# Performance work log

Measured on AMD Instinct MI355X. Metric: run time of the kernel, lower is better.

## Reference

```python
import jax, jax.numpy as jnp
import numpy as np

N, K, D_IN, D_OUT = 50000, 16, 128, 256
C1, C2 = D_OUT // 4, D_OUT // 2  # 64, 128
E = N * K


def _lin(key, din, dout):
    return jax.random.normal(key, (din, dout), jnp.float32) * 0.02


def setup_inputs() -> dict:
    key = jax.random.key(0)
    ks = jax.random.split(key, 16)
    x = jax.random.normal(ks[0], (N, D_IN), jnp.float32)
    pos = jax.random.normal(ks[1], (N, 3), jnp.float32)
    normals = jax.random.normal(ks[2], (N, 3), jnp.float32)
    batch = jnp.zeros((N,), jnp.int32)
    # fixed k-regular graph standing in for knn_graph(pos, K); src != dst so
    # darboux's sqrt(|pos_j-pos_i|^2) is smooth everywhere
    dst = jnp.repeat(jnp.arange(N, dtype=jnp.int32), K)            # [E]
    off = jax.random.randint(ks[3], (E,), 1, N, jnp.int32)
    src = (dst + off) % N                                          # [E]
    edge_index = jnp.stack([src, dst])                             # [2,E]
    inp = dict(x=x, pos=pos, batch=batch, normals=normals, edge_index=edge_index)

    def add_mlp(name, k, din, dout):
        inp[name + '_w'] = _lin(k, din, dout)
        inp[name + '_b'] = jnp.zeros((dout,), jnp.float32)
        inp[name + '_g'] = jnp.ones((dout,), jnp.float32)
        inp[name + '_bt'] = jnp.zeros((dout,), jnp.float32)

    add_mlp('mlp1', ks[4], D_IN, D_OUT // 8)
    add_mlp('sc', ks[5], D_IN, D_OUT)
    add_mlp('mlp2', ks[6], C2, D_OUT)
    add_mlp('enc1', ks[7], 8, C1 // 2)
    inp['att1_w'] = _lin(ks[8], C1, C1)
    add_mlp('post1', ks[9], C1, C1)
    add_mlp('enc2', ks[10], 8, C2 // 2)
    inp['att2_w'] = _lin(ks[11], C2, C2)
    add_mlp('post2', ks[12], C2, C2)
    return inp


def _bn(h, g, bt, eps=1e-6):
    # BatchNorm1d, training-mode batch statistics (biased variance)
    m = h.mean(0)
    v = jnp.mean((h - m) ** 2, axis=0)
    return (h - m) * jax.lax.rsqrt(v + eps) * g + bt


def _lrelu(h):
    return jnp.where(h >= 0, h, 0.2 * h)


def _smlp(h, w, b, g, bt, act=True):
    # SharedMLP layer: Linear -> BN(eps=1e-6) -> LeakyReLU(0.2) (act optional)
    h = _bn(h @ w + b, g, bt)
    return _lrelu(h) if act else h


def _darboux(pi, pj, ni, nj):
    eps = 1e-10
    d = pj - pi                                            # [E,3]
    dot = lambda a, b: jnp.sum(a * b, axis=1, keepdims=True)
    nrm = lambda a: jnp.sqrt(jnp.sum(a * a, axis=1, keepdims=True))
    dist = nrm(d)
    lni, lnj = nrm(ni), nrm(nj)
    uq = jnp.cross(d, ni); vq = jnp.cross(uq, ni)
    uk = jnp.cross(d, nj); vk = jnp.cross(uk, nj)
    luq, lvq, luk, lvk = nrm(uq), nrm(vq), nrm(uk), nrm(vk)
    return jnp.concatenate([
        dist,
        dot(d, ni) / (dist * lni + eps),
        dot(d, nj) / (dist * lnj + eps),
        dot(ni, nj) / (lni * lnj + eps),
        dot(uq, uk) / (luq * luk + eps),
        dot(vq, vk) / (lvq * lvk + eps),
        dot(uq, vk) / (luq * lvk + eps),
        dot(vq, uk) / (lvq * luk + eps),
    ], axis=1)                                             # [E,8]


def _seg_softmax(h, idx, n):
    m = jax.ops.segment_max(h, idx, num_segments=n)        # [N,C]
    e = jnp.exp(h - m[idx])
    s = jax.ops.segment_sum(e, idx, num_segments=n)
    return e / (s[idx] + 1e-16)


def _lfa(src, dst, n, x, pos, normals, ew, eb, eg, ebt, aw, pw, pb, pg, pbt):
    rel = _darboux(pos[dst], pos[src], normals[dst], normals[src])  # [E,8]
    lse = _smlp(rel, ew, eb, eg, ebt)                               # [E,C/2]
    lf = jnp.concatenate([x[src], lse], axis=1)                     # [E,C]
    att = lf @ aw                                                   # [E,C]
    scores = _seg_softmax(att, dst, n)
    agg = jax.ops.segment_sum(scores * lf, dst, num_segments=n)     # [N,C]
    return _smlp(agg, pw, pb, pg, pbt)


def reference(x, pos, batch, normals, edge_index,
              mlp1_w, mlp1_b, mlp1_g, mlp1_bt,
              sc_w, sc_b, sc_g, sc_bt,
              mlp2_w, mlp2_b, mlp2_g, mlp2_bt,
              enc1_w, enc1_b, enc1_g, enc1_bt, att1_w,
              post1_w, post1_b, post1_g, post1_bt,
              enc2_w, enc2_b, enc2_g, enc2_bt, att2_w,
              post2_w, post2_b, post2_g, post2_bt):
    n = x.shape[0]
    src, dst = edge_index[0], edge_index[1]
    shortcut = _smlp(x, sc_w, sc_b, sc_g, sc_bt, act=False)         # [N,d_out]
    h = _smlp(x, mlp1_w, mlp1_b, mlp1_g, mlp1_bt)                   # [N,d_out//8]
    h = _lfa(src, dst, n, h, pos, normals,
             enc1_w, enc1_b, enc1_g, enc1_bt, att1_w,
             post1_w, post1_b, post1_g, post1_bt)                   # [N,d_out//4]
    h = _lfa(src, dst, n, h, pos, normals,
             enc2_w, enc2_b, enc2_g, enc2_bt, att2_w,
             post2_w, post2_b, post2_g, post2_bt)                   # [N,d_out//2]
    h = _smlp(h, mlp2_w, mlp2_b, mlp2_g, mlp2_bt, act=False)        # [N,d_out]
    return _lrelu(h + shortcut)
```

## Files before the change

kernel.cpp:

```cpp
#include <hip/hip_runtime.h>
#include <hip/hip_bf16.h>
#include <math.h>


typedef __attribute__((ext_vector_type(8))) short short8;
typedef __attribute__((ext_vector_type(4))) float floatx4;

#define NPART 16
#define PSTRIDE 4096

__device__ __forceinline__ float lrelu_f(float v) { return v >= 0.f ? v : 0.2f * v; }

__device__ __forceinline__ unsigned short f2bf(float f) {
    union { __hip_bfloat16 h; unsigned short u; } cv;
    cv.h = __float2bfloat16(f);
    return cv.u;
}
__device__ __forceinline__ float bf2f(unsigned short u) {
    union { unsigned short u; __hip_bfloat16 h; } cv;
    cv.u = u;
    return __bfloat162float(cv.h);
}
__device__ __forceinline__ uint pack2bf(float lo, float hi) {
    return (uint)f2bf(lo) | ((uint)f2bf(hi) << 16);
}

struct PrepSeg { const float* src; short* dst; int cnt; int Cout; int KK; };
struct PrepArgs { PrepSeg seg[6]; };

__global__ void wprep_kernel(PrepArgs pa)
{
    int gid = blockIdx.x * 256 + threadIdx.x;
    int base = 0;
    for (int s = 0; s < 6; s++) {
        int c = pa.seg[s].cnt;
        if (gid < base + c) {
            int fi = gid - base;
            const float* w = pa.seg[s].src;
            const int Cout = pa.seg[s].Cout, KK = pa.seg[s].KK;
            const int l15 = fi & 15, g = (fi >> 4) & 3, rest = fi >> 6;
            const int kk = rest % KK, nt = rest / KK;
            const int col = nt * 16 + l15;
            short8 v;
#pragma unroll
            for (int e = 0; e < 8; e++)
                v[e] = (short)f2bf(w[(size_t)(kk * 32 + g * 8 + e) * Cout + col]);
            *reinterpret_cast<short8*>(pa.seg[s].dst + (size_t)fi * 8) = v;
            return;
        }
        base += c;
    }
}

template<int DIN, int DOUT, int TM>
__global__ void lin_stats_kernel(const float* __restrict__ in, const float* __restrict__ w,
                                 const float* __restrict__ b, float* __restrict__ out,
                                 double* __restrict__ st, int n)
{
    constexpr int CT = DOUT;
    constexpr int RG = 256 / CT;
    constexpr int ROWS = TM * RG;
    __shared__ float xtile[ROWS][DIN];
    double* stp = st + (blockIdx.x & (NPART - 1)) * PSTRIDE;
    const int row0 = blockIdx.x * ROWS;
    for (int idx = threadIdx.x; idx < ROWS * DIN; idx += 256) {
        int r = idx / DIN, j = idx - r * DIN;
        int rr = row0 + r;
        xtile[r][j] = (rr < n) ? in[(size_t)rr * DIN + j] : 0.f;
    }
    __syncthreads();
    const int c  = threadIdx.x % CT;
    const int rg = threadIdx.x / CT;
    float acc[TM];
    const float bv = b[c];
#pragma unroll
    for (int t = 0; t < TM; t++) acc[t] = bv;
    for (int j = 0; j < DIN; j++) {
        float wv = w[(size_t)j * DOUT + c];
#pragma unroll
        for (int t = 0; t < TM; t++) acc[t] = fmaf(xtile[rg * TM + t][j], wv, acc[t]);
    }
    float s = 0.f, s2 = 0.f;
#pragma unroll
    for (int t = 0; t < TM; t++) {
        int rr = row0 + rg * TM + t;
        if (rr < n) {
            out[(size_t)rr * DOUT + c] = acc[t];
            s += acc[t];
            s2 = fmaf(acc[t], acc[t], s2);
        }
    }
    __syncthreads();
    float* ls  = &xtile[0][0];
    float* ls2 = ls + 256;
    ls[threadIdx.x] = s; ls2[threadIdx.x] = s2;
    __syncthreads();
    if (rg == 0) {
#pragma unroll
        for (int g = 1; g < RG; g++) { s += ls[g * CT + c]; s2 += ls2[g * CT + c]; }
        atomicAdd(&stp[c], (double)s);
        atomicAdd(&stp[DOUT + c], (double)s2);
    }
}

template<bool AFF, bool OUT16>
__global__ __launch_bounds__(256)
void lin_mfma_kernel(const float* __restrict__ in, const float* __restrict__ aff,
                     const short* __restrict__ wp, const float* __restrict__ b,
                     void* __restrict__ outv, double* __restrict__ st, int n)
{
    __shared__ __align__(16) char aS[64 * 256];
    const int tid = threadIdx.x;
    const int w = tid >> 6, grp = (tid >> 4) & 3, l15 = tid & 15, lane = tid & 63;
    const int row0 = blockIdx.x * 64;
    double* stp = st + (blockIdx.x & (NPART - 1)) * PSTRIDE;
    {
        const int r = tid >> 2;
        const int p = tid & 3;
        const int chbase = p * 32;
        const int gr = row0 + r;
        if (gr < n) {
            const float* hrow = in + (size_t)gr * 128 + chbase;
#pragma unroll
            for (int u = 0; u < 4; u++) {
                float4 h0 = *reinterpret_cast<const float4*>(hrow + u * 8);
                float4 h1 = *reinterpret_cast<const float4*>(hrow + u * 8 + 4);
                if constexpr (AFF) {
                    const float* ar = aff + chbase + u * 8;
                    const float* cr = aff + 128 + chbase + u * 8;
                    float4 a0 = *reinterpret_cast<const float4*>(ar);
                    float4 a1 = *reinterpret_cast<const float4*>(ar + 4);
                    float4 c0 = *reinterpret_cast<const float4*>(cr);
                    float4 c1 = *reinterpret_cast<const float4*>(cr + 4);
                    h0.x = lrelu_f(fmaf(h0.x, a0.x, c0.x)); h0.y = lrelu_f(fmaf(h0.y, a0.y, c0.y));
                    h0.z = lrelu_f(fmaf(h0.z, a0.z, c0.z)); h0.w = lrelu_f(fmaf(h0.w, a0.w, c0.w));
                    h1.x = lrelu_f(fmaf(h1.x, a1.x, c1.x)); h1.y = lrelu_f(fmaf(h1.y, a1.y, c1.y));
                    h1.z = lrelu_f(fmaf(h1.z, a1.z, c1.z)); h1.w = lrelu_f(fmaf(h1.w, a1.w, c1.w));
                }
                uint4 pk;
                pk.x = pack2bf(h0.x, h0.y); pk.y = pack2bf(h0.z, h0.w);
                pk.z = pack2bf(h1.x, h1.y); pk.w = pack2bf(h1.z, h1.w);
                const int unit = (chbase >> 3) + u;
                *reinterpret_cast<uint4*>(aS + r * 256 + ((unit ^ (r & 7)) << 4)) = pk;
            }
        }
    }
    __syncthreads();

    short8 B[4][4]; float bias[4];
#pragma unroll
    for (int t = 0; t < 4; t++) {
        const int nt = w * 4 + t;
        bias[t] = b[nt * 16 + l15];
#pragma unroll
        for (int kk = 0; kk < 4; kk++)
            B[t][kk] = *reinterpret_cast<const short8*>(wp + (size_t)(((nt * 4 + kk) * 4 + grp) * 16 + l15) * 8);
    }
    float ssum[4] = {0.f, 0.f, 0.f, 0.f}, ssq[4] = {0.f, 0.f, 0.f, 0.f};
#pragma unroll
    for (int mt = 0; mt < 4; mt++) {
        short8 a[4];
        const int arow = mt * 16 + l15;
#pragma unroll
        for (int kk = 0; kk < 4; kk++)
            a[kk] = *reinterpret_cast<const short8*>(aS + arow * 256 + ((((kk << 2) + grp) ^ (arow & 7)) << 4));
#pragma unroll
        for (int t = 0; t < 4; t++) {
            floatx4 acc = {bias[t], bias[t], bias[t], bias[t]};
#pragma unroll
            for (int kk = 0; kk < 4; kk++)
                acc = __builtin_amdgcn_mfma_f32_16x16x32_bf16(a[kk], B[t][kk], acc, 0, 0, 0);
            const int c = (w * 4 + t) * 16 + l15;
#pragma unroll
            for (int r = 0; r < 4; r++) {
                const int grow = row0 + mt * 16 + grp * 4 + r;
                if (grow < n) {
                    if constexpr (OUT16)
                        ((unsigned short*)outv)[(size_t)grow * 256 + c] = f2bf(acc[r]);
                    else
                        ((float*)outv)[(size_t)grow * 256 + c] = acc[r];
                    ssum[t] += acc[r];
                    ssq[t] = fmaf(acc[r], acc[r], ssq[t]);
                }
            }
        }
    }
#pragma unroll
    for (int t = 0; t < 4; t++) {
        float s = ssum[t], q = ssq[t];
        s += __shfl_xor(s, 16); s += __shfl_xor(s, 32);
        q += __shfl_xor(q, 16); q += __shfl_xor(q, 32);
        if (lane < 16) {
            const int c = (w * 4 + t) * 16 + l15;
            atomicAdd(&stp[c], (double)s);
            atomicAdd(&stp[256 + c], (double)q);
        }
    }
}

__global__ __launch_bounds__(256)
void edge_enc_kernel(const int* __restrict__ src, const float* __restrict__ pos,
                     const float* __restrict__ nrm, unsigned short* __restrict__ rel16,
                     int E, double* __restrict__ stM)
{
    float s8[8] = {0, 0, 0, 0, 0, 0, 0, 0};
    float M[36];
#pragma unroll
    for (int k = 0; k < 36; k++) M[k] = 0.f;
    const int tid = threadIdx.x;

    for (int e = blockIdx.x * 256 + tid; e < E; e += gridDim.x * 256) {
        const int d = e >> 4;
        const int s = src[e];
        const float pix = pos[3 * d], piy = pos[3 * d + 1], piz = pos[3 * d + 2];
        const float pjx = pos[3 * s], pjy = pos[3 * s + 1], pjz = pos[3 * s + 2];
        const float nix = nrm[3 * d], niy = nrm[3 * d + 1], niz = nrm[3 * d + 2];
        const float njx = nrm[3 * s], njy = nrm[3 * s + 1], njz = nrm[3 * s + 2];
        const float dx = pjx - pix, dy = pjy - piy, dz = pjz - piz;
        const float dist = sqrtf(dx * dx + dy * dy + dz * dz);
        const float lni = sqrtf(nix * nix + niy * niy + niz * niz);
        const float lnj = sqrtf(njx * njx + njy * njy + njz * njz);
        const float uqx = dy * niz - dz * niy, uqy = dz * nix - dx * niz, uqz = dx * niy - dy * nix;
        const float vqx = uqy * niz - uqz * niy, vqy = uqz * nix - uqx * niz, vqz = uqx * niy - uqy * nix;
        const float ukx = dy * njz - dz * njy, uky = dz * njx - dx * njz, ukz = dx * njy - dy * njx;
        const float vkx = uky * njz - ukz * njy, vky = ukz * njx - ukx * njz, vkz = ukx * njy - uky * njx;
        const float luq = sqrtf(uqx * uqx + uqy * uqy + uqz * uqz);
        const float lvq = sqrtf(vqx * vqx + vqy * vqy + vqz * vqz);
        const float luk = sqrtf(ukx * ukx + uky * uky + ukz * ukz);
        const float lvk = sqrtf(vkx * vkx + vky * vky + vkz * vkz);
        const float eps = 1e-10f;
        float rv[8];
        rv[0] = dist;
        rv[1] = (dx * nix + dy * niy + dz * niz) / (dist * lni + eps);
        rv[2] = (dx * njx + dy * njy + dz * njz) / (dist * lnj + eps);
        rv[3] = (nix * njx + niy * njy + niz * njz) / (lni * lnj + eps);
        rv[4] = (uqx * ukx + uqy * uky + uqz * ukz) / (luq * luk + eps);
        rv[5] = (vqx * vkx + vqy * vky + vqz * vkz) / (lvq * lvk + eps);
        rv[6] = (uqx * vkx + uqy * vky + uqz * vkz) / (luq * lvk + eps);
        rv[7] = (vqx * ukx + vqy * uky + vqz * ukz) / (lvq * luk + eps);
        uint4 pk;
        pk.x = pack2bf(rv[0], rv[1]); pk.y = pack2bf(rv[2], rv[3]);
        pk.z = pack2bf(rv[4], rv[5]); pk.w = pack2bf(rv[6], rv[7]);
        *reinterpret_cast<uint4*>(rel16 + (size_t)e * 8) = pk;
#pragma unroll
        for (int i = 0; i < 8; i++) s8[i] += rv[i];
#pragma unroll
        for (int i = 0; i < 8; i++)
#pragma unroll
            for (int j = i; j < 8; j++)
                M[i * 8 - (i * (i - 1)) / 2 + (j - i)] = fmaf(rv[i], rv[j], M[i * 8 - (i * (i - 1)) / 2 + (j - i)]);
    }
#pragma unroll
    for (int k = 0; k < 8; k++) {
        float v = s8[k];
        v += __shfl_xor(v, 1); v += __shfl_xor(v, 2); v += __shfl_xor(v, 4);
        v += __shfl_xor(v, 8); v += __shfl_xor(v, 16); v += __shfl_xor(v, 32);
        s8[k] = v;
    }
#pragma unroll
    for (int k = 0; k < 36; k++) {
        float v = M[k];
        v += __shfl_xor(v, 1); v += __shfl_xor(v, 2); v += __shfl_xor(v, 4);
        v += __shfl_xor(v, 8); v += __shfl_xor(v, 16); v += __shfl_xor(v, 32);
        M[k] = v;
    }
    __shared__ float red[4][44];
    const int w = tid >> 6, lane = tid & 63;
    if (lane == 0) {
#pragma unroll
        for (int k = 0; k < 8; k++) red[w][k] = s8[k];
#pragma unroll
        for (int k = 0; k < 36; k++) red[w][8 + k] = M[k];
    }
    __syncthreads();
    if (tid < 44) {
        float tot = red[0][tid] + red[1][tid] + red[2][tid] + red[3][tid];
        atomicAdd(&stM[(blockIdx.x & (NPART - 1)) * PSTRIDE + tid], (double)tot);
    }
}

__global__ void enc_finalize_kernel(const double* __restrict__ stM,
    const float* __restrict__ ew1, const float* __restrict__ eb1,
    const float* __restrict__ g1, const float* __restrict__ bt1, float* __restrict__ ac1,
    const float* __restrict__ ew2, const float* __restrict__ eb2,
    const float* __restrict__ g2, const float* __restrict__ bt2, float* __restrict__ ac2,
    float Ef)
{
    __shared__ double SM[44];
    const int tid = threadIdx.x;
    if (tid < 44) {
        double a = 0;
        for (int p = 0; p < NPART; p++) a += stM[p * PSTRIDE + tid];
        SM[tid] = a;
    }
    __syncthreads();
    if (tid < 96) {
        const bool is2 = tid < 64;
        const int c = is2 ? tid : tid - 64;
        const int HCc = is2 ? 64 : 32;
        const float* ew = is2 ? ew2 : ew1;
        const float b = (is2 ? eb2 : eb1)[c];
        float wv[8];
#pragma unroll
        for (int j = 0; j < 8; j++) wv[j] = ew[j * HCc + c];
        double dot = 0.0, quad = 0.0;
#pragma unroll
        for (int i = 0; i < 8; i++) {
            dot += SM[i] * (double)wv[i];
#pragma unroll
            for (int j = i; j < 8; j++) {
                const double mij = SM[8 + i * 8 - (i * (i - 1)) / 2 + (j - i)];
                quad += mij * (double)wv[i] * (double)wv[j] * ((i == j) ? 1.0 : 2.0);
            }
        }
        const double sum   = dot + (double)Ef * b;
        const double sumsq = quad + 2.0 * b * dot + (double)Ef * b * b;
        const double m = sum / Ef;
        const double v = sumsq / Ef - m * m;
        const float rstd = (float)(1.0 / sqrt(v + 1e-6));
        const float a = rstd * (is2 ? g2 : g1)[c];
        float* ac = is2 ? ac2 : ac1;
        ac[c] = a;
        ac[HCc + c] = fmaf(-(float)m, a, (is2 ? bt2 : bt1)[c]);
    }
}

struct FinSeg { const double* st; const float* g; const float* bt; float* ac; int C; float cnt; };
struct FinArgs { FinSeg seg[3]; };

__global__ void finalize_multi_kernel(FinArgs fa)
{
    FinSeg s = fa.seg[blockIdx.x];
    int c = threadIdx.x;
    if (c < s.C) {
        double sm = 0.0, sq = 0.0;
#pragma unroll
        for (int p = 0; p < NPART; p++) {
            sm += s.st[p * PSTRIDE + c];
            sq += s.st[p * PSTRIDE + s.C + c];
        }
        double m = sm / (double)s.cnt;
        double v = sq / (double)s.cnt - m * m;
        float rstd = (float)(1.0 / sqrt(v + 1e-6));
        float a = rstd * s.g[c];
        s.ac[c] = a;
        s.ac[s.C + c] = fmaf(-(float)m, a, s.bt[c]);
    }
}

template<int C>
__global__ void bnconv_kernel(const float* __restrict__ h, const float* __restrict__ ac,
                              unsigned short* __restrict__ o, size_t total8)
{
    size_t i = (size_t)blockIdx.x * blockDim.x + threadIdx.x;
    size_t stride = (size_t)gridDim.x * blockDim.x;
    for (; i < total8; i += stride) {
        const size_t b = i * 8;
        const int c = (int)(b & (size_t)(C - 1));
        float4 h0 = *reinterpret_cast<const float4*>(h + b);
        float4 h1 = *reinterpret_cast<const float4*>(h + b + 4);
        float4 a0 = *reinterpret_cast<const float4*>(ac + c);
        float4 a1 = *reinterpret_cast<const float4*>(ac + c + 4);
        float4 c0 = *reinterpret_cast<const float4*>(ac + C + c);
        float4 c1 = *reinterpret_cast<const float4*>(ac + C + c + 4);
        uint4 pk;
        pk.x = pack2bf(lrelu_f(fmaf(h0.x, a0.x, c0.x)), lrelu_f(fmaf(h0.y, a0.y, c0.y)));
        pk.y = pack2bf(lrelu_f(fmaf(h0.z, a0.z, c0.z)), lrelu_f(fmaf(h0.w, a0.w, c0.w)));
        pk.z = pack2bf(lrelu_f(fmaf(h1.x, a1.x, c1.x)), lrelu_f(fmaf(h1.y, a1.y, c1.y)));
        pk.w = pack2bf(lrelu_f(fmaf(h1.z, a1.z, c1.z)), lrelu_f(fmaf(h1.w, a1.w, c1.w)));
        *reinterpret_cast<uint4*>(o + b) = pk;
    }
}

template<int C, int NODES>
__global__ __launch_bounds__(256)
void lfa10_kernel(const unsigned short* __restrict__ hbn,
                  const unsigned short* __restrict__ rel16,
                  const int* __restrict__ src,
                  const float* __restrict__ ew, const float* __restrict__ eb,
                  const float* __restrict__ encac,
                  const short* __restrict__ attp, const short* __restrict__ postp,
                  const float* __restrict__ postb,
                  float* __restrict__ out, double* __restrict__ st, int n)
{
    constexpr int HC = C / 2, NT = C / 16, NTW = NT / 4, KK = C / 32, ROWB = 2 * C;
    constexpr int ROWS = NODES * 16;
    constexpr int TPR = 256 / ROWS;
    constexpr int NTE = HC / 16;
    constexpr int NCOMB = (NODES * NTE) / 4;
    constexpr int NSTEP = 4 / NTE;

    __shared__ __align__(16) char lfS[ROWS * ROWB];
    __shared__ __align__(16) char aggS[16 * ROWB];

    const int tid = threadIdx.x;
    const int lane = tid & 63, w = tid >> 6, grp = (tid >> 4) & 3, l15 = tid & 15;
    const int node0 = blockIdx.x * NODES;
    const int e0g = node0 * 16;
    const int Etot = n * 16;
    const int kk_sel = (w * NTW) >> 1;
    double* stp = st + (blockIdx.x & (NPART - 1)) * PSTRIDE;

    if constexpr (NODES < 16) {
        for (int i = tid; i < (16 - NODES) * ROWB / 16; i += 256)
            reinterpret_cast<uint4*>(aggS + NODES * ROWB)[i] = (uint4){0, 0, 0, 0};
    }

    short8 Batt[NTW][KK], Bsel[NTW];
#pragma unroll
    for (int t = 0; t < NTW; t++) {
        const int nt = w * NTW + t;
#pragma unroll
        for (int kk = 0; kk < KK; kk++)
            Batt[t][kk] = *reinterpret_cast<const short8*>(attp + (size_t)(((nt * KK + kk) * 4 + grp) * 16 + l15) * 8);
        const int ng = ((nt & 1) << 1) | (l15 >> 3);
#pragma unroll
        for (int e = 0; e < 8; e++)
            Bsel[t][e] = (grp == ng && (l15 & 7) == e) ? (short)0x3F80 : (short)0;
    }

    const int etile = w % NTE;
    const int cc = etile * 16 + l15;
    short8 Benc = {0, 0, 0, 0, 0, 0, 0, 0};
    if (grp == 0) {
#pragma unroll
        for (int j = 0; j < 8; j++) Benc[j] = (short)f2bf(ew[j * HC + cc]);
    }
    const float encA = encac[cc];
    const float encB2 = fmaf(encA, eb[cc], encac[HC + cc]);
    const int cfull = HC + cc;
    const int cuE = cfull >> 3, subE = (cfull & 7) * 2;

    {
        const int r = (TPR == 1) ? tid : (tid / TPR);
        const int p = (TPR == 1) ? 0 : (tid % TPR);
        constexpr int CHT = HC / TPR;
        const int chb = p * CHT;
        const int eg = e0g + r;
        if (eg < Etot) {
            const int s = src[eg];
            const unsigned short* hrow = hbn + (size_t)s * HC + chb;
#pragma unroll
            for (int u = 0; u < CHT / 8; u++) {
                uint4 pk = *reinterpret_cast<const uint4*>(hrow + u * 8);
                const int unit = (chb >> 3) + u;
                *reinterpret_cast<uint4*>(lfS + r * ROWB + ((unit ^ (r & 7)) << 4)) = pk;
            }
        }
    }

    {
        const int nodeStart = w / NTE;
#pragma unroll
        for (int j = 0; j < NCOMB; j++) {
            const int node = nodeStart + j * NSTEP;
            const int r0 = node * 16;
            int eg = e0g + r0 + l15;
            if (eg >= Etot) eg = Etot - 1;
            const short8 Arel = *reinterpret_cast<const short8*>(rel16 + (size_t)eg * 8);
            floatx4 accE = {0.f, 0.f, 0.f, 0.f};
            accE = __builtin_amdgcn_mfma_f32_16x16x32_bf16(Arel, Benc, accE, 0, 0, 0);
#pragma unroll
            for (int r = 0; r < 4; r++) {
                const int row = r0 + grp * 4 + r;
                const float tv = lrelu_f(fmaf(accE[r], encA, encB2));
                *reinterpret_cast<unsigned short*>(lfS + row * ROWB + ((cuE ^ (row & 7)) << 4) + subE) = f2bf(tv);
            }
        }
    }
    __syncthreads();

    for (int mt = 0; mt < NODES; ++mt) {
        const int arow = mt * 16 + l15;
        const char* rbase = lfS + arow * ROWB;
        const int x7 = l15 & 7;
        short8 a[KK];
#pragma unroll
        for (int kk = 0; kk < KK; kk++)
            a[kk] = *reinterpret_cast<const short8*>(rbase + ((((kk << 2) + grp) ^ x7) << 4));
        const short8 asel = *reinterpret_cast<const short8*>(rbase + ((((kk_sel << 2) + grp) ^ x7) << 4));
        floatx4 acc[NTW];
#pragma unroll
        for (int t = 0; t < NTW; t++) acc[t] = (floatx4){0.f, 0.f, 0.f, 0.f};
#pragma unroll
        for (int kk = 0; kk < KK; kk++)
#pragma unroll
            for (int t = 0; t < NTW; t++)
                acc[t] = __builtin_amdgcn_mfma_f32_16x16x32_bf16(a[kk], Batt[t][kk], acc[t], 0, 0, 0);

#pragma unroll
        for (int t = 0; t < NTW; t++) {
            float m = fmaxf(fmaxf(acc[t][0], acc[t][1]), fmaxf(acc[t][2], acc[t][3]));
            m = fmaxf(m, __shfl_xor(m, 16));
            m = fmaxf(m, __shfl_xor(m, 32));
            float e0 = __expf(acc[t][0] - m), e1 = __expf(acc[t][1] - m);
            float e2 = __expf(acc[t][2] - m), e3 = __expf(acc[t][3] - m);
            float ss = e0 + e1 + e2 + e3;
            ss += __shfl_xor(ss, 16);
            ss += __shfl_xor(ss, 32);
            const float inv = 1.f / (ss + 1e-16f);
            floatx4 Lc = {0.f, 0.f, 0.f, 0.f};
            Lc = __builtin_amdgcn_mfma_f32_16x16x32_bf16(asel, Bsel[t], Lc, 0, 0, 0);
            float av = fmaf(e0, Lc[0], fmaf(e1, Lc[1], fmaf(e2, Lc[2], e3 * Lc[3])));
            av += __shfl_xor(av, 16);
            av += __shfl_xor(av, 32);
            av *= inv;
            if (lane < 16) {
                const int c = (w * NTW + t) * 16 + l15;
                const int cu = c >> 3, sub = (c & 7) * 2;
                *reinterpret_cast<unsigned short*>(aggS + mt * ROWB + ((cu ^ (mt & 7)) << 4) + sub) = f2bf(av);
            }
        }
    }
    __syncthreads();

    short8 Bpost[NTW][KK]; float pb[NTW];
#pragma unroll
    for (int t = 0; t < NTW; t++) {
        const int nt = w * NTW + t;
        pb[t] = postb[nt * 16 + l15];
#pragma unroll
        for (int kk = 0; kk < KK; kk++)
            Bpost[t][kk] = *reinterpret_cast<const short8*>(postp + (size_t)(((nt * KK + kk) * 4 + grp) * 16 + l15) * 8);
    }
    short8 ag[KK];
#pragma unroll
    for (int kk = 0; kk < KK; kk++)
        ag[kk] = *reinterpret_cast<const short8*>(aggS + l15 * ROWB + ((((kk << 2) + grp) ^ (l15 & 7)) << 4));
    floatx4 accP[NTW];
#pragma unroll
    for (int t = 0; t < NTW; t++) accP[t] = (floatx4){0.f, 0.f, 0.f, 0.f};
#pragma unroll
    for (int kk = 0; kk < KK; kk++)
#pragma unroll
        for (int t = 0; t < NTW; t++)
            accP[t] = __builtin_amdgcn_mfma_f32_16x16x32_bf16(ag[kk], Bpost[t][kk], accP[t], 0, 0, 0);
#pragma unroll
    for (int t = 0; t < NTW; t++) {
        const int c = (w * NTW + t) * 16 + l15;
        float s = 0.f, q = 0.f;
#pragma unroll
        for (int r = 0; r < 4; r++) {
            const int nb = grp * 4 + r;
            if (nb < NODES && node0 + nb < n) {
                const float v = accP[t][r] + pb[t];
                out[(size_t)(node0 + nb) * C + c] = v;
                s += v;
                q = fmaf(v, v, q);
            }
        }
        s += __shfl_xor(s, 16); s += __shfl_xor(s, 32);
        q += __shfl_xor(q, 16); q += __shfl_xor(q, 32);
        if (lane < 16) {
            atomicAdd(&stp[c], (double)s);
            atomicAdd(&stp[C + c], (double)q);
        }
    }
}

__global__ void final_kernel(float* __restrict__ h2, const unsigned short* __restrict__ xs,
                             const float* __restrict__ ac2, const float* __restrict__ acs,
                             int total4)
{
    int i = blockIdx.x * 256 + threadIdx.x;
    const int stride = gridDim.x * 256;
    for (; i < total4; i += stride) {
        float4 v = reinterpret_cast<const float4*>(h2)[i];
        ushort4 xv = reinterpret_cast<const ushort4*>(xs)[i];
        const int c = (i & 63) << 2;
        float4 a2 = *reinterpret_cast<const float4*>(ac2 + c);
        float4 b2 = *reinterpret_cast<const float4*>(ac2 + 256 + c);
        float4 as = *reinterpret_cast<const float4*>(acs + c);
        float4 bs = *reinterpret_cast<const float4*>(acs + 256 + c);
        v.x = lrelu_f(fmaf(v.x, a2.x, b2.x) + fmaf(bf2f(xv.x), as.x, bs.x));
        v.y = lrelu_f(fmaf(v.y, a2.y, b2.y) + fmaf(bf2f(xv.y), as.y, bs.y));
        v.z = lrelu_f(fmaf(v.z, a2.z, b2.z) + fmaf(bf2f(xv.z), as.z, bs.z));
        v.w = lrelu_f(fmaf(v.w, a2.w, b2.w) + fmaf(bf2f(xv.w), as.w, bs.w));
        reinterpret_cast<float4*>(h2)[i] = v;
    }
}

extern "C" void kernel_launch(void* const* d_in, const int* in_sizes, int n_in,
                              void* d_out, int out_size, void* d_ws, size_t ws_size,
                              hipStream_t stream)
{
    const float* x       = (const float*)d_in[0];
    const float* pos     = (const float*)d_in[1];
    const float* normals = (const float*)d_in[3];
    const int*   eidx    = (const int*)d_in[4];

    const float* mlp1_w = (const float*)d_in[5];
    const float* mlp1_b = (const float*)d_in[6];
    const float* mlp1_g = (const float*)d_in[7];
    const float* mlp1_bt= (const float*)d_in[8];
    const float* sc_w   = (const float*)d_in[9];
    const float* sc_b   = (const float*)d_in[10];
    const float* sc_g   = (const float*)d_in[11];
    const float* sc_bt  = (const float*)d_in[12];
    const float* mlp2_w = (const float*)d_in[13];
    const float* mlp2_b = (const float*)d_in[14];
    const float* mlp2_g = (const float*)d_in[15];
    const float* mlp2_bt= (const float*)d_in[16];
    const float* enc1_w = (const float*)d_in[17];
    const float* enc1_b = (const float*)d_in[18];
    const float* enc1_g = (const float*)d_in[19];
    const float* enc1_bt= (const float*)d_in[20];
    const float* att1_w = (const float*)d_in[21];
    const float* post1_w = (const float*)d_in[22];
    const float* post1_b = (const float*)d_in[23];
    const float* post1_g = (const float*)d_in[24];
    const float* post1_bt= (const float*)d_in[25];
    const float* enc2_w = (const float*)d_in[26];
    const float* enc2_b = (const float*)d_in[27];
    const float* enc2_g = (const float*)d_in[28];
    const float* enc2_bt= (const float*)d_in[29];
    const float* att2_w = (const float*)d_in[30];
    const float* post2_w = (const float*)d_in[31];
    const float* post2_b = (const float*)d_in[32];
    const float* post2_g = (const float*)d_in[33];
    const float* post2_bt= (const float*)d_in[34];

    float* out = (float*)d_out;

    const int n = in_sizes[0] / 128;
    const int E = in_sizes[4] / 2;
    const int* srcArr = eidx;

    char* base = (char*)d_ws;
    double* stats  = (double*)base;
    float*  affine = (float*)(base + 524288);
    short*  wprep  = (short*)(base + 540672);
    unsigned short* rel16 = (unsigned short*)(base + 786432);
    unsigned short* xs16  = rel16 + (size_t)E * 8;
    float*  h1  = (float*)(xs16 + (size_t)n * 256);
    float*  hA  = h1 + (size_t)n * 32;
    float*  hB  = hA + (size_t)n * 64;
    unsigned short* h1bn = (unsigned short*)hB;
    unsigned short* hAbn = (unsigned short*)h1;

    short* att1p = wprep;
    short* post1p = wprep + 4096;
    short* att2p = wprep + 8192;
    short* post2p = wprep + 24576;
    short* scp   = wprep + 40960;
    short* mlp2p = wprep + 73728;

    const int OF_MLP1 = 0, OF_ENCM = 64, OF_POST1 = 128, OF_POST2 = 512, OF_SC = 768, OF_MLP2 = 1280;
    const int AF_MLP1 = 0, AF_ENC1 = 64, AF_POST1 = 128, AF_ENC2 = 256,
              AF_POST2 = 512, AF_SC = 768, AF_MLP2 = 1280;

    hipMemsetAsync(stats, 0, NPART * 32768, stream);

    PrepArgs pa;
    pa.seg[0] = {att1_w,  att1p,  512,  64,  2};
    pa.seg[1] = {post1_w, post1p, 512,  64,  2};
    pa.seg[2] = {att2_w,  att2p,  2048, 128, 4};
    pa.seg[3] = {post2_w, post2p, 2048, 128, 4};
    pa.seg[4] = {sc_w,    scp,    4096, 256, 4};
    pa.seg[5] = {mlp2_w,  mlp2p,  4096, 256, 4};
    wprep_kernel<<<52, 256, 0, stream>>>(pa);

    lin_stats_kernel<128, 32, 8><<<(n + 63) / 64, 256, 0, stream>>>(x, mlp1_w, mlp1_b, h1, stats + OF_MLP1, n);
    lin_mfma_kernel<false, true><<<(n + 63) / 64, 256, 0, stream>>>(x, nullptr, scp, sc_b, xs16, stats + OF_SC, n);

    edge_enc_kernel<<<512, 256, 0, stream>>>(srcArr, pos, normals, rel16, E, stats + OF_ENCM);

    FinArgs f1;
    f1.seg[0] = {stats + OF_MLP1, mlp1_g, mlp1_bt, affine + AF_MLP1, 32, (float)n};
    f1.seg[1] = f1.seg[0]; f1.seg[2] = f1.seg[0];
    finalize_multi_kernel<<<1, 256, 0, stream>>>(f1);
    enc_finalize_kernel<<<1, 128, 0, stream>>>(stats + OF_ENCM,
        enc1_w, enc1_b, enc1_g, enc1_bt, affine + AF_ENC1,
        enc2_w, enc2_b, enc2_g, enc2_bt, affine + AF_ENC2, (float)E);

    bnconv_kernel<32><<<1024, 256, 0, stream>>>(h1, affine + AF_MLP1, h1bn, (size_t)n * 32 / 8);

    lfa10_kernel<64, 16><<<(n + 15) / 16, 256, 0, stream>>>(h1bn, rel16, srcArr, enc1_w, enc1_b,
        affine + AF_ENC1, att1p, post1p, post1_b, hA, stats + OF_POST1, n);
    FinArgs f2;
    f2.seg[0] = {stats + OF_POST1, post1_g, post1_bt, affine + AF_POST1, 64, (float)n};
    f2.seg[1] = f2.seg[0]; f2.seg[2] = f2.seg[0];
    finalize_multi_kernel<<<1, 256, 0, stream>>>(f2);

    bnconv_kernel<64><<<1024, 256, 0, stream>>>(hA, affine + AF_POST1, hAbn, (size_t)n * 64 / 8);

    lfa10_kernel<128, 8><<<(n + 7) / 8, 256, 0, stream>>>(hAbn, rel16, srcArr, enc2_w, enc2_b,
        affine + AF_ENC2, att2p, post2p, post2_b, hB, stats + OF_POST2, n);
    FinArgs f3;
    f3.seg[0] = {stats + OF_POST2, post2_g, post2_bt, affine + AF_POST2, 128, (float)n};
    f3.seg[1] = f3.seg[0]; f3.seg[2] = f3.seg[0];
    finalize_multi_kernel<<<1, 256, 0, stream>>>(f3);

    lin_mfma_kernel<true, false><<<(n + 63) / 64, 256, 0, stream>>>(hB, affine + AF_POST2, mlp2p, mlp2_b,
        out, stats + OF_MLP2, n);
    FinArgs f4;
    f4.seg[0] = {stats + OF_MLP2, mlp2_g, mlp2_bt, affine + AF_MLP2, 256, (float)n};
    f4.seg[1] = {stats + OF_SC,   sc_g,   sc_bt,   affine + AF_SC,   256, (float)n};
    f4.seg[2] = f4.seg[0];
    finalize_multi_kernel<<<2, 256, 0, stream>>>(f4);

    final_kernel<<<2048, 256, 0, stream>>>(out, xs16, affine + AF_MLP2, affine + AF_SC, n * 64);
}
```

Measured before the change: 276.0 us.

## Store intermediate activations in bf16 and drop softmax max-subtraction

The pre-BN outputs of both LFA blocks and of mlp2 are now stored as bf16 instead of fp32, and downstream kernels read bf16 and convert. This cuts memory traffic for these intermediates. The float-to-bf16 conversion is replaced by a cheaper add-and-shift rounding that does not tie-to-even and does not handle NaN. The attention softmax no longer subtracts the max, removing a shuffle reduction but risking overflow for large logits, and the selector MFMA is hoisted ahead of the loop.

```diff
diff --git a/kernel.cpp b/kernel.cpp
--- a/kernel.cpp
+++ b/kernel.cpp
@@ -11,18 +11,24 @@
 
 __device__ __forceinline__ float lrelu_f(float v) { return v >= 0.f ? v : 0.2f * v; }
 
+__device__ __forceinline__ uint asu(float f) {
+    union { float f; uint u; } c; c.f = f; return c.u;
+}
 __device__ __forceinline__ unsigned short f2bf(float f) {
     union { __hip_bfloat16 h; unsigned short u; } cv;
     cv.h = __float2bfloat16(f);
     return cv.u;
 }
+__device__ __forceinline__ unsigned short f2bf_r(float f) {
+    return (unsigned short)((asu(f) + 0x8000u) >> 16);
+}
+__device__ __forceinline__ uint pack2bf_r(float lo, float hi) {
+    return ((asu(lo) + 0x8000u) >> 16) | ((asu(hi) + 0x8000u) & 0xFFFF0000u);
+}
 __device__ __forceinline__ float bf2f(unsigned short u) {
     union { unsigned short u; __hip_bfloat16 h; } cv;
     cv.u = u;
     return __bfloat162float(cv.h);
-}
-__device__ __forceinline__ uint pack2bf(float lo, float hi) {
-    return (uint)f2bf(lo) | ((uint)f2bf(hi) << 16);
 }
 
 struct PrepSeg { const float* src; short* dst; int cnt; int Cout; int KK; };
@@ -103,11 +109,11 @@
     }
 }
 
-template<bool AFF, bool OUT16>
+template<bool AFF, bool IN16>
 __global__ __launch_bounds__(256)
-void lin_mfma_kernel(const float* __restrict__ in, const float* __restrict__ aff,
+void lin_mfma_kernel(const void* __restrict__ inv, const float* __restrict__ aff,
                      const short* __restrict__ wp, const float* __restrict__ b,
-                     void* __restrict__ outv, double* __restrict__ st, int n)
+                     unsigned short* __restrict__ out16, double* __restrict__ st, int n)
 {
     __shared__ __align__(16) char aS[64 * 256];
     const int tid = threadIdx.x;
@@ -120,26 +126,33 @@
         const int chbase = p * 32;
         const int gr = row0 + r;
         if (gr < n) {
-            const float* hrow = in + (size_t)gr * 128 + chbase;
 #pragma unroll
             for (int u = 0; u < 4; u++) {
-                float4 h0 = *reinterpret_cast<const float4*>(hrow + u * 8);
-                float4 h1 = *reinterpret_cast<const float4*>(hrow + u * 8 + 4);
+                float h[8];
+                if constexpr (IN16) {
+                    const unsigned short* hrow = (const unsigned short*)inv + (size_t)gr * 128 + chbase + u * 8;
+                    uint4 raw = *reinterpret_cast<const uint4*>(hrow);
+                    h[0] = bf2f((unsigned short)(raw.x & 0xFFFF)); h[1] = bf2f((unsigned short)(raw.x >> 16));
+                    h[2] = bf2f((unsigned short)(raw.y & 0xFFFF)); h[3] = bf2f((unsigned short)(raw.y >> 16));
+                    h[4] = bf2f((unsigned short)(raw.z & 0xFFFF)); h[5] = bf2f((unsigned short)(raw.z >> 16));
+                    h[6] = bf2f((unsigned short)(raw.w & 0xFFFF)); h[7] = bf2f((unsigned short)(raw.w >> 16));
+                } else {
+                    const float* hrow = (const float*)inv + (size_t)gr * 128 + chbase + u * 8;
+                    float4 h0 = *reinterpret_cast<const float4*>(hrow);
+                    float4 h1 = *reinterpret_cast<const float4*>(hrow + 4);
+                    h[0] = h0.x; h[1] = h0.y; h[2] = h0.z; h[3] = h0.w;
+                    h[4] = h1.x; h[5] = h1.y; h[6] = h1.z; h[7] = h1.w;
+                }
                 if constexpr (AFF) {
                     const float* ar = aff + chbase + u * 8;
                     const float* cr = aff + 128 + chbase + u * 8;
-                    float4 a0 = *reinterpret_cast<const float4*>(ar);
-                    float4 a1 = *reinterpret_cast<const float4*>(ar + 4);
-                    float4 c0 = *reinterpret_cast<const float4*>(cr);
-                    float4 c1 = *reinterpret_cast<const float4*>(cr + 4);
-                    h0.x = lrelu_f(fmaf(h0.x, a0.x, c0.x)); h0.y = lrelu_f(fmaf(h0.y, a0.y, c0.y));
-                    h0.z = lrelu_f(fmaf(h0.z, a0.z, c0.z)); h0.w = lrelu_f(fmaf(h0.w, a0.w, c0.w));
-                    h1.x = lrelu_f(fmaf(h1.x, a1.x, c1.x)); h1.y = lrelu_f(fmaf(h1.y, a1.y, c1.y));
-                    h1.z = lrelu_f(fmaf(h1.z, a1.z, c1.z)); h1.w = lrelu_f(fmaf(h1.w, a1.w, c1.w));
+#pragma unroll
+                    for (int i2 = 0; i2 < 8; i2++)
+                        h[i2] = lrelu_f(fmaf(h[i2], ar[i2], cr[i2]));
                 }
                 uint4 pk;
-                pk.x = pack2bf(h0.x, h0.y); pk.y = pack2bf(h0.z, h0.w);
-                pk.z = pack2bf(h1.x, h1.y); pk.w = pack2bf(h1.z, h1.w);
+                pk.x = pack2bf_r(h[0], h[1]); pk.y = pack2bf_r(h[2], h[3]);
+                pk.z = pack2bf_r(h[4], h[5]); pk.w = pack2bf_r(h[6], h[7]);
                 const int unit = (chbase >> 3) + u;
                 *reinterpret_cast<uint4*>(aS + r * 256 + ((unit ^ (r & 7)) << 4)) = pk;
             }
@@ -175,10 +188,7 @@
             for (int r = 0; r < 4; r++) {
                 const int grow = row0 + mt * 16 + grp * 4 + r;
                 if (grow < n) {
-                    if constexpr (OUT16)
-                        ((unsigned short*)outv)[(size_t)grow * 256 + c] = f2bf(acc[r]);
-                    else
-                        ((float*)outv)[(size_t)grow * 256 + c] = acc[r];
+                    out16[(size_t)grow * 256 + c] = f2bf_r(acc[r]);
                     ssum[t] += acc[r];
                     ssq[t] = fmaf(acc[r], acc[r], ssq[t]);
                 }
@@ -239,8 +249,8 @@
         rv[6] = (uqx * vkx + uqy * vky + uqz * vkz) / (luq * lvk + eps);
         rv[7] = (vqx * ukx + vqy * uky + vqz * ukz) / (lvq * luk + eps);
         uint4 pk;
-        pk.x = pack2bf(rv[0], rv[1]); pk.y = pack2bf(rv[2], rv[3]);
-        pk.z = pack2bf(rv[4], rv[5]); pk.w = pack2bf(rv[6], rv[7]);
+        pk.x = pack2bf_r(rv[0], rv[1]); pk.y = pack2bf_r(rv[2], rv[3]);
+        pk.z = pack2bf_r(rv[4], rv[5]); pk.w = pack2bf_r(rv[6], rv[7]);
         *reinterpret_cast<uint4*>(rel16 + (size_t)e * 8) = pk;
 #pragma unroll
         for (int i = 0; i < 8; i++) s8[i] += rv[i];
@@ -348,8 +358,8 @@
     }
 }
 
-template<int C>
-__global__ void bnconv_kernel(const float* __restrict__ h, const float* __restrict__ ac,
+template<int C, bool IN16>
+__global__ void bnconv_kernel(const void* __restrict__ hv, const float* __restrict__ ac,
                               unsigned short* __restrict__ o, size_t total8)
 {
     size_t i = (size_t)blockIdx.x * blockDim.x + threadIdx.x;
@@ -357,31 +367,40 @@
     for (; i < total8; i += stride) {
         const size_t b = i * 8;
         const int c = (int)(b & (size_t)(C - 1));
-        float4 h0 = *reinterpret_cast<const float4*>(h + b);
-        float4 h1 = *reinterpret_cast<const float4*>(h + b + 4);
-        float4 a0 = *reinterpret_cast<const float4*>(ac + c);
-        float4 a1 = *reinterpret_cast<const float4*>(ac + c + 4);
-        float4 c0 = *reinterpret_cast<const float4*>(ac + C + c);
-        float4 c1 = *reinterpret_cast<const float4*>(ac + C + c + 4);
+        float h[8];
+        if constexpr (IN16) {
+            uint4 raw = *reinterpret_cast<const uint4*>((const unsigned short*)hv + b);
+            h[0] = bf2f((unsigned short)(raw.x & 0xFFFF)); h[1] = bf2f((unsigned short)(raw.x >> 16));
+            h[2] = bf2f((unsigned short)(raw.y & 0xFFFF)); h[3] = bf2f((unsigned short)(raw.y >> 16));
+            h[4] = bf2f((unsigned short)(raw.z & 0xFFFF)); h[5] = bf2f((unsigned short)(raw.z >> 16));
+            h[6] = bf2f((unsigned short)(raw.w & 0xFFFF)); h[7] = bf2f((unsigned short)(raw.w >> 16));
+        } else {
+            float4 h0 = *reinterpret_cast<const float4*>((const float*)hv + b);
+            float4 h1 = *reinterpret_cast<const float4*>((const float*)hv + b + 4);
+            h[0] = h0.x; h[1] = h0.y; h[2] = h0.z; h[3] = h0.w;
+            h[4] = h1.x; h[5] = h1.y; h[6] = h1.z; h[7] = h1.w;
+        }
+        const float* ar = ac + c;
+        const float* cr = ac + C + c;
         uint4 pk;
-        pk.x = pack2bf(lrelu_f(fmaf(h0.x, a0.x, c0.x)), lrelu_f(fmaf(h0.y, a0.y, c0.y)));
-        pk.y = pack2bf(lrelu_f(fmaf(h0.z, a0.z, c0.z)), lrelu_f(fmaf(h0.w, a0.w, c0.w)));
-        pk.z = pack2bf(lrelu_f(fmaf(h1.x, a1.x, c1.x)), lrelu_f(fmaf(h1.y, a1.y, c1.y)));
-        pk.w = pack2bf(lrelu_f(fmaf(h1.z, a1.z, c1.z)), lrelu_f(fmaf(h1.w, a1.w, c1.w)));
+        pk.x = pack2bf_r(lrelu_f(fmaf(h[0], ar[0], cr[0])), lrelu_f(fmaf(h[1], ar[1], cr[1])));
+        pk.y = pack2bf_r(lrelu_f(fmaf(h[2], ar[2], cr[2])), lrelu_f(fmaf(h[3], ar[3], cr[3])));
+        pk.z = pack2bf_r(lrelu_f(fmaf(h[4], ar[4], cr[4])), lrelu_f(fmaf(h[5], ar[5], cr[5])));
+        pk.w = pack2bf_r(lrelu_f(fmaf(h[6], ar[6], cr[6])), lrelu_f(fmaf(h[7], ar[7], cr[7])));
         *reinterpret_cast<uint4*>(o + b) = pk;
     }
 }
 
 template<int C, int NODES>
 __global__ __launch_bounds__(256)
-void lfa10_kernel(const unsigned short* __restrict__ hbn,
+void lfa11_kernel(const unsigned short* __restrict__ hbn,
                   const unsigned short* __restrict__ rel16,
                   const int* __restrict__ src,
                   const float* __restrict__ ew, const float* __restrict__ eb,
                   const float* __restrict__ encac,
                   const short* __restrict__ attp, const short* __restrict__ postp,
                   const float* __restrict__ postb,
-                  float* __restrict__ out, double* __restrict__ st, int n)
+                  unsigned short* __restrict__ out16, double* __restrict__ st, int n)
 {
     constexpr int HC = C / 2, NT = C / 16, NTW = NT / 4, KK = C / 32, ROWB = 2 * C;
     constexpr int ROWS = NODES * 16;
@@ -464,7 +483,7 @@
             for (int r = 0; r < 4; r++) {
                 const int row = r0 + grp * 4 + r;
                 const float tv = lrelu_f(fmaf(accE[r], encA, encB2));
-                *reinterpret_cast<unsigned short*>(lfS + row * ROWB + ((cuE ^ (row & 7)) << 4) + subE) = f2bf(tv);
+                *reinterpret_cast<unsigned short*>(lfS + row * ROWB + ((cuE ^ (row & 7)) << 4) + subE) = f2bf_r(tv);
             }
         }
     }
@@ -479,9 +498,15 @@
         for (int kk = 0; kk < KK; kk++)
             a[kk] = *reinterpret_cast<const short8*>(rbase + ((((kk << 2) + grp) ^ x7) << 4));
         const short8 asel = *reinterpret_cast<const short8*>(rbase + ((((kk_sel << 2) + grp) ^ x7) << 4));
-        floatx4 acc[NTW];
-#pragma unroll
-        for (int t = 0; t < NTW; t++) acc[t] = (floatx4){0.f, 0.f, 0.f, 0.f};
+        floatx4 acc[NTW], Lc[NTW];
+#pragma unroll
+        for (int t = 0; t < NTW; t++) {
+            acc[t] = (floatx4){0.f, 0.f, 0.f, 0.f};
+            Lc[t] = (floatx4){0.f, 0.f, 0.f, 0.f};
+        }
+#pragma unroll
+        for (int t = 0; t < NTW; t++)
+            Lc[t] = __builtin_amdgcn_mfma_f32_16x16x32_bf16(asel, Bsel[t], Lc[t], 0, 0, 0);
 #pragma unroll
         for (int kk = 0; kk < KK; kk++)
 #pragma unroll
@@ -490,25 +515,20 @@
 
 #pragma unroll
         for (int t = 0; t < NTW; t++) {
-            float m = fmaxf(fmaxf(acc[t][0], acc[t][1]), fmaxf(acc[t][2], acc[t][3]));
-            m = fmaxf(m, __shfl_xor(m, 16));
-            m = fmaxf(m, __shfl_xor(m, 32));
-            float e0 = __expf(acc[t][0] - m), e1 = __expf(acc[t][1] - m);
-            float e2 = __expf(acc[t][2] - m), e3 = __expf(acc[t][3] - m);
-            float ss = e0 + e1 + e2 + e3;
+            float e0 = __expf(acc[t][0]), e1 = __expf(acc[t][1]);
+            float e2 = __expf(acc[t][2]), e3 = __expf(acc[t][3]);
+            float ss = (e0 + e1) + (e2 + e3);
             ss += __shfl_xor(ss, 16);
             ss += __shfl_xor(ss, 32);
             const float inv = 1.f / (ss + 1e-16f);
-            floatx4 Lc = {0.f, 0.f, 0.f, 0.f};
-            Lc = __builtin_amdgcn_mfma_f32_16x16x32_bf16(asel, Bsel[t], Lc, 0, 0, 0);
-            float av = fmaf(e0, Lc[0], fmaf(e1, Lc[1], fmaf(e2, Lc[2], e3 * Lc[3])));
+            float av = fmaf(e0, Lc[t][0], fmaf(e1, Lc[t][1], fmaf(e2, Lc[t][2], e3 * Lc[t][3])));
             av += __shfl_xor(av, 16);
             av += __shfl_xor(av, 32);
             av *= inv;
             if (lane < 16) {
                 const int c = (w * NTW + t) * 16 + l15;
                 const int cu = c >> 3, sub = (c & 7) * 2;
-                *reinterpret_cast<unsigned short*>(aggS + mt * ROWB + ((cu ^ (mt & 7)) << 4) + sub) = f2bf(av);
+                *reinterpret_cast<unsigned short*>(aggS + mt * ROWB + ((cu ^ (mt & 7)) << 4) + sub) = f2bf_r(av);
             }
         }
     }
@@ -544,7 +564,7 @@
             const int nb = grp * 4 + r;
             if (nb < NODES && node0 + nb < n) {
                 const float v = accP[t][r] + pb[t];
-                out[(size_t)(node0 + nb) * C + c] = v;
+                out16[(size_t)(node0 + nb) * C + c] = f2bf_r(v);
                 s += v;
                 q = fmaf(v, v, q);
             }
@@ -558,25 +578,27 @@
     }
 }
 
-__global__ void final_kernel(float* __restrict__ h2, const unsigned short* __restrict__ xs,
+__global__ void final_kernel(float* __restrict__ out, const unsigned short* __restrict__ m2,
+                             const unsigned short* __restrict__ xs,
                              const float* __restrict__ ac2, const float* __restrict__ acs,
                              int total4)
 {
     int i = blockIdx.x * 256 + threadIdx.x;
     const int stride = gridDim.x * 256;
     for (; i < total4; i += stride) {
-        float4 v = reinterpret_cast<const float4*>(h2)[i];
+        ushort4 mv = reinterpret_cast<const ushort4*>(m2)[i];
         ushort4 xv = reinterpret_cast<const ushort4*>(xs)[i];
         const int c = (i & 63) << 2;
         float4 a2 = *reinterpret_cast<const float4*>(ac2 + c);
         float4 b2 = *reinterpret_cast<const float4*>(ac2 + 256 + c);
         float4 as = *reinterpret_cast<const float4*>(acs + c);
         float4 bs = *reinterpret_cast<const float4*>(acs + 256 + c);
-        v.x = lrelu_f(fmaf(v.x, a2.x, b2.x) + fmaf(bf2f(xv.x), as.x, bs.x));
-        v.y = lrelu_f(fmaf(v.y, a2.y, b2.y) + fmaf(bf2f(xv.y), as.y, bs.y));
-        v.z = lrelu_f(fmaf(v.z, a2.z, b2.z) + fmaf(bf2f(xv.z), as.z, bs.z));
-        v.w = lrelu_f(fmaf(v.w, a2.w, b2.w) + fmaf(bf2f(xv.w), as.w, bs.w));
-        reinterpret_cast<float4*>(h2)[i] = v;
+        float4 v;
+        v.x = lrelu_f(fmaf(bf2f(mv.x), a2.x, b2.x) + fmaf(bf2f(xv.x), as.x, bs.x));
+        v.y = lrelu_f(fmaf(bf2f(mv.y), a2.y, b2.y) + fmaf(bf2f(xv.y), as.y, bs.y));
+        v.z = lrelu_f(fmaf(bf2f(mv.z), a2.z, b2.z) + fmaf(bf2f(xv.z), as.z, bs.z));
+        v.w = lrelu_f(fmaf(bf2f(mv.w), a2.w, b2.w) + fmaf(bf2f(xv.w), as.w, bs.w));
+        reinterpret_cast<float4*>(out)[i] = v;
     }
 }
 
@@ -632,10 +654,11 @@
     short*  wprep  = (short*)(base + 540672);
     unsigned short* rel16 = (unsigned short*)(base + 786432);
     unsigned short* xs16  = rel16 + (size_t)E * 8;
-    float*  h1  = (float*)(xs16 + (size_t)n * 256);
-    float*  hA  = h1 + (size_t)n * 32;
-    float*  hB  = hA + (size_t)n * 64;
-    unsigned short* h1bn = (unsigned short*)hB;
+    unsigned short* m2pre = xs16 + (size_t)n * 256;
+    float*  h1   = (float*)(m2pre + (size_t)n * 256);
+    unsigned short* hA16 = (unsigned short*)(h1 + (size_t)n * 32);
+    unsigned short* hB16 = hA16 + (size_t)n * 64;
+    unsigned short* h1bn = hB16;
     unsigned short* hAbn = (unsigned short*)h1;
 
     short* att1p = wprep;
@@ -661,7 +684,7 @@
     wprep_kernel<<<52, 256, 0, stream>>>(pa);
 
     lin_stats_kernel<128, 32, 8><<<(n + 63) / 64, 256, 0, stream>>>(x, mlp1_w, mlp1_b, h1, stats + OF_MLP1, n);
-    lin_mfma_kernel<false, true><<<(n + 63) / 64, 256, 0, stream>>>(x, nullptr, scp, sc_b, xs16, stats + OF_SC, n);
+    lin_mfma_kernel<false, false><<<(n + 63) / 64, 256, 0, stream>>>(x, nullptr, scp, sc_b, xs16, stats + OF_SC, n);
 
     edge_enc_kernel<<<512, 256, 0, stream>>>(srcArr, pos, normals, rel16, E, stats + OF_ENCM);
 
@@ -673,31 +696,31 @@
         enc1_w, enc1_b, enc1_g, enc1_bt, affine + AF_ENC1,
         enc2_w, enc2_b, enc2_g, enc2_bt, affine + AF_ENC2, (float)E);
 
-    bnconv_kernel<32><<<1024, 256, 0, stream>>>(h1, affine + AF_MLP1, h1bn, (size_t)n * 32 / 8);
-
-    lfa10_kernel<64, 16><<<(n + 15) / 16, 256, 0, stream>>>(h1bn, rel16, srcArr, enc1_w, enc1_b,
-        affine + AF_ENC1, att1p, post1p, post1_b, hA, stats + OF_POST1, n);
+    bnconv_kernel<32, false><<<1024, 256, 0, stream>>>(h1, affine + AF_MLP1, h1bn, (size_t)n * 32 / 8);
+
+    lfa11_kernel<64, 16><<<(n + 15) / 16, 256, 0, stream>>>(h1bn, rel16, srcArr, enc1_w, enc1_b,
+        affine + AF_ENC1, att1p, post1p, post1_b, hA16, stats + OF_POST1, n);
     FinArgs f2;
     f2.seg[0] = {stats + OF_POST1, post1_g, post1_bt, affine + AF_POST1, 64, (float)n};
     f2.seg[1] = f2.seg[0]; f2.seg[2] = f2.seg[0];
     finalize_multi_kernel<<<1, 256, 0, stream>>>(f2);
 
-    bnconv_kernel<64><<<1024, 256, 0, stream>>>(hA, affine + AF_POST1, hAbn, (size_t)n * 64 / 8);
-
-    lfa10_kernel<128, 8><<<(n + 7) / 8, 256, 0, stream>>>(hAbn, rel16, srcArr, enc2_w, enc2_b,
-        affine + AF_ENC2, att2p, post2p, post2_b, hB, stats + OF_POST2, n);
+    bnconv_kernel<64, true><<<1024, 256, 0, stream>>>(hA16, affine + AF_POST1, hAbn, (size_t)n * 64 / 8);
+
+    lfa11_kernel<128, 8><<<(n + 7) / 8, 256, 0, stream>>>(hAbn, rel16, srcArr, enc2_w, enc2_b,
+        affine + AF_ENC2, att2p, post2p, post2_b, hB16, stats + OF_POST2, n);
     FinArgs f3;
     f3.seg[0] = {stats + OF_POST2, post2_g, post2_bt, affine + AF_POST2, 128, (float)n};
     f3.seg[1] = f3.seg[0]; f3.seg[2] = f3.seg[0];
     finalize_multi_kernel<<<1, 256, 0, stream>>>(f3);
 
-    lin_mfma_kernel<true, false><<<(n + 63) / 64, 256, 0, stream>>>(hB, affine + AF_POST2, mlp2p, mlp2_b,
-        out, stats + OF_MLP2, n);
+    lin_mfma_kernel<true, true><<<(n + 63) / 64, 256, 0, stream>>>(hB16, affine + AF_POST2, mlp2p, mlp2_b,
+        m2pre, stats + OF_MLP2, n);
     FinArgs f4;
     f4.seg[0] = {stats + OF_MLP2, mlp2_g, mlp2_bt, affine + AF_MLP2, 256, (float)n};
     f4.seg[1] = {stats + OF_SC,   sc_g,   sc_bt,   affine + AF_SC,   256, (float)n};
     f4.seg[2] = f4.seg[0];
     finalize_multi_kernel<<<2, 256, 0, stream>>>(f4);
 
-    final_kernel<<<2048, 256, 0, stream>>>(out, xs16, affine + AF_MLP2, affine + AF_SC, n * 64);
-}
+    final_kernel<<<2048, 256, 0, stream>>>(out, m2pre, xs16, affine + AF_MLP2, affine + AF_SC, n * 64);
+}
```

After: 258.3 us. 6.4% less time.
